# Kernel tuning notes

Hardware: AMD Instinct MI355X
Metric: run time of the kernel (lower is better)

The kernel has to match this reference:

```python
import jax, jax.numpy as jnp
import numpy as np

B, S, IN, H, E, OUT = 64, 2048, 256, 512, 256, 32000


def setup_inputs() -> dict:
    key = jax.random.key(0)
    ks = jax.random.split(key, 20)
    g = lambda k, shp, fan_in: jax.random.normal(k, shp, jnp.float32) / jnp.sqrt(jnp.float32(fan_in))
    return {
        "x": jax.random.normal(ks[0], (B, IN), jnp.float32),
        "hidden": jax.random.normal(ks[1], (B, H), jnp.float32),
        "encoder_outputs": jax.random.normal(ks[2], (B, S, H), jnp.float32),
        # attention params
        "W1_w": g(ks[3], (H, E), H), "W1_b": jnp.zeros((E,), jnp.float32),
        "W2_w": g(ks[4], (H, E), H),
        "v_w": g(ks[5], (E, 1), E),
        # GRU gate params (input to gates is concat(x, context): IN+H)
        "Wxr_w": g(ks[6], (IN + H, H), IN + H), "Wxr_b": jnp.zeros((H,), jnp.float32),
        "Whr_w": g(ks[7], (H, H), H),
        "Wxz_w": g(ks[8], (IN + H, H), IN + H), "Wxz_b": jnp.zeros((H,), jnp.float32),
        "Whz_w": g(ks[9], (H, H), H),
        "Wxh_w": g(ks[10], (IN + H, H), IN + H), "Wxh_b": jnp.zeros((H,), jnp.float32),
        "Whh_w": g(ks[11], (H, H), H),
        # output projection
        "Who_w": g(ks[12], (H, OUT), H), "Who_b": jnp.zeros((OUT,), jnp.float32),
    }


def reference(x, hidden, encoder_outputs,
              W1_w, W1_b, W2_w, v_w,
              Wxr_w, Wxr_b, Whr_w,
              Wxz_w, Wxz_b, Whz_w,
              Wxh_w, Wxh_b, Whh_w,
              Who_w, Who_b):
    # Bahdanau attention
    # energy: [B, S, E]
    energy = jnp.tanh(jnp.einsum("bsh,he->bse", encoder_outputs, W1_w) + W1_b
                      + (hidden @ W2_w)[:, None, :])
    scores = jnp.einsum("bse,eo->bs", energy, v_w)          # [B, S]
    attn_weights = jax.nn.softmax(scores, axis=1)            # [B, S]
    context = jnp.einsum("bs,bsh->bh", attn_weights, encoder_outputs)  # [B, H]

    x_context = jnp.concatenate([x, context], axis=-1)       # [B, IN+H]
    reset_gate = jax.nn.sigmoid(x_context @ Wxr_w + Wxr_b + hidden @ Whr_w)
    update_gate = jax.nn.sigmoid(x_context @ Wxz_w + Wxz_b + hidden @ Whz_w)
    h_tilde = jnp.tanh(x_context @ Wxh_w + Wxh_b + (reset_gate * hidden) @ Whh_w)
    new_hidden = update_gate * hidden + (1.0 - update_gate) * h_tilde
    output = new_hidden @ Who_w + Who_b                      # [B, OUT]
    return (output, new_hidden, attn_weights)
```

## Files before the change

### kernel.cpp

```cpp
#include <hip/hip_runtime.h>

#define BB 64
#define SS 2048
#define INDIM 256
#define HH 512
#define EE 256
#define OUTD 32000

typedef __attribute__((ext_vector_type(8))) short short8;
typedef __attribute__((ext_vector_type(4))) float floatx4;

#define LOG2E 1.4426950408889634f

__device__ __forceinline__ unsigned short f2bf(float f) {
  unsigned u = __float_as_uint(f);
  return (unsigned short)((u + 0x7FFFu + ((u >> 16) & 1u)) >> 16);
}
__device__ __forceinline__ unsigned pk2(float a, float b) {
  return (unsigned)f2bf(a) | ((unsigned)f2bf(b) << 16);
}
__device__ __forceinline__ float bf2f(unsigned short u) {
  return __uint_as_float((unsigned)u << 16);
}
__device__ __forceinline__ float fast_tanh(float x) {
  float e = __builtin_amdgcn_exp2f(x * 2.8853900817779268f);
  return 1.0f - 2.0f * __builtin_amdgcn_rcpf(e + 1.0f);
}
__device__ __forceinline__ float fast_sigmoid(float x) {
  float e = __builtin_amdgcn_exp2f(-x * LOG2E);
  return __builtin_amdgcn_rcpf(1.0f + e);
}

#define WS_W1T   0
#define WS_HBP   262144
#define WS_CTX   393216
#define WS_NHBF  524288
#define WS_Z     589824
#define WS_RH    720896
#define WS_GP    851968
#define WS_NP    3473408
#define WS_CTXP  4784128
#define WS_SUMP  38338560

__global__ void k_prep(const float* __restrict__ W1, unsigned short* __restrict__ W1t) {
  int idx = blockIdx.x * 256 + threadIdx.x;
  int k = idx >> 8, e = idx & 255;
  W1t[e * HH + k] = f2bf(W1[idx]);
}

__global__ __launch_bounds__(256) void k_hb(const float* __restrict__ hidden,
                                            const float* __restrict__ W2,
                                            const float* __restrict__ W1b,
                                            float* __restrict__ hbp) {
  int b0 = blockIdx.x * 4, seg = blockIdx.y, e = threadIdx.x;
  int h0 = seg * 256;
  float a0 = 0, a1 = 0, a2 = 0, a3 = 0;
  if (seg == 0) { a0 = a1 = a2 = a3 = W1b[e]; }
  for (int h = 0; h < 256; ++h) {
    float w = W2[(h0 + h) * EE + e];
    a0 += hidden[(b0 + 0) * HH + h0 + h] * w;
    a1 += hidden[(b0 + 1) * HH + h0 + h] * w;
    a2 += hidden[(b0 + 2) * HH + h0 + h] * w;
    a3 += hidden[(b0 + 3) * HH + h0 + h] * w;
  }
  float* o = hbp + (size_t)seg * BB * EE;
  o[(b0 + 0) * EE + e] = a0; o[(b0 + 1) * EE + e] = a1;
  o[(b0 + 2) * EE + e] = a2; o[(b0 + 3) * EE + e] = a3;
}

#define LDA 520
__global__ __launch_bounds__(256, 4) void k_scores(
    const float* __restrict__ enc, const unsigned short* __restrict__ W1t,
    const float* __restrict__ hbp, const float* __restrict__ vw,
    float* __restrict__ attn, float* __restrict__ ctxp, float* __restrict__ sump) {
  __shared__ unsigned short Afull[32 * LDA];
  __shared__ float hb_s[EE], v_s[EE];
  __shared__ float red[4 * 32];
  __shared__ float wbuf[32];

  int tid = threadIdx.x;
  int m0 = blockIdx.x * 32;
  int b = blockIdx.x >> 6;
  int sloc = (blockIdx.x & 63) * 32;
  hb_s[tid] = hbp[b * EE + tid] + hbp[BB * EE + b * EE + tid];
  v_s[tid] = vw[tid];

  int lane = tid & 63, wn = tid >> 6;
  int l15 = lane & 15, quad = lane >> 4;

  int row0 = tid >> 3, kg = tid & 7;
  const float* base0 = enc + (size_t)(m0 + row0) * HH + kg * 4;

  floatx4 acc[2][4];
#pragma unroll
  for (int i = 0; i < 2; ++i)
#pragma unroll
    for (int j = 0; j < 4; ++j) acc[i][j] = (floatx4)0.0f;

  float4 pf[6];
#pragma unroll
  for (int d = 0; d < 6; ++d) pf[d] = *(const float4*)(base0 + d * 32);

  short8 bcur[4];
#pragma unroll
  for (int j = 0; j < 4; ++j)
    bcur[j] = *(const short8*)(W1t + (wn * 64 + j * 16 + l15) * HH + quad * 8);

#pragma unroll
  for (int kb = 0; kb < 16; ++kb) {
    int slot = kb % 6;
    {
      float4 f = pf[slot];
      uint2 w; w.x = pk2(f.x, f.y); w.y = pk2(f.z, f.w);
      *(uint2*)(Afull + row0 * LDA + kb * 32 + kg * 4) = w;
    }
    if (kb + 6 < 16) pf[slot] = *(const float4*)(base0 + (kb + 6) * 32);
    short8 bnx[4];
    if (kb + 1 < 16) {
      int kkn = (kb + 1) * 32 + quad * 8;
#pragma unroll
      for (int j = 0; j < 4; ++j)
        bnx[j] = *(const short8*)(W1t + (wn * 64 + j * 16 + l15) * HH + kkn);
    }
    asm volatile("s_waitcnt lgkmcnt(0)" ::: "memory");
    __builtin_amdgcn_s_barrier();
    int kk = kb * 32 + quad * 8;
    short8 a0v = *(const short8*)(Afull + l15 * LDA + kk);
    short8 a1v = *(const short8*)(Afull + (16 + l15) * LDA + kk);
#pragma unroll
    for (int j = 0; j < 4; ++j) {
      acc[0][j] = __builtin_amdgcn_mfma_f32_16x16x32_bf16(a0v, bcur[j], acc[0][j], 0, 0, 0);
      acc[1][j] = __builtin_amdgcn_mfma_f32_16x16x32_bf16(a1v, bcur[j], acc[1][j], 0, 0, 0);
    }
    if (kb + 1 < 16) {
#pragma unroll
      for (int j = 0; j < 4; ++j) bcur[j] = bnx[j];
    }
  }
  __syncthreads();

#pragma unroll
  for (int i = 0; i < 2; ++i)
#pragma unroll
    for (int r = 0; r < 4; ++r) {
      float s = 0.0f;
#pragma unroll
      for (int j = 0; j < 4; ++j) {
        int e = wn * 64 + j * 16 + l15;
        s += fast_tanh(acc[i][j][r] + hb_s[e]) * v_s[e];
      }
#pragma unroll
      for (int off = 1; off < 16; off <<= 1) s += __shfl_xor(s, off, 64);
      if (l15 == 0) red[wn * 32 + i * 16 + quad * 4 + r] = s;
    }
  __syncthreads();
  if (tid < 32) {
    float sc = red[tid] + red[32 + tid] + red[64 + tid] + red[96 + tid];
    float e = __builtin_amdgcn_exp2f(sc * LOG2E);
    wbuf[tid] = e;
    attn[b * SS + sloc + tid] = e;
    float s = e;
#pragma unroll
    for (int off = 1; off < 32; off <<= 1) s += __shfl_xor(s, off, 64);
    if (tid == 0) sump[blockIdx.x] = s;
  }
  __syncthreads();

  float cacc[8];
#pragma unroll
  for (int j = 0; j < 8; ++j) cacc[j] = 0.0f;
#pragma unroll
  for (int rr = 0; rr < 8; ++rr) {
    int r = wn * 8 + rr;
    float w = wbuf[r];
    short8 av = *(const short8*)(Afull + r * LDA + lane * 8);
#pragma unroll
    for (int j = 0; j < 8; ++j) cacc[j] += w * bf2f((unsigned short)av[j]);
  }
  float4 c0, c1;
  c0.x = cacc[0]; c0.y = cacc[1]; c0.z = cacc[2]; c0.w = cacc[3];
  c1.x = cacc[4]; c1.y = cacc[5]; c1.z = cacc[6]; c1.w = cacc[7];
  float* cp = ctxp + ((size_t)blockIdx.x * 4 + wn) * HH + lane * 8;
  *(float4*)cp = c0;
  *(float4*)(cp + 4) = c1;
}

__global__ __launch_bounds__(512) void k_norm(float* __restrict__ attn,
                                              const float* __restrict__ ctxp,
                                              const float* __restrict__ sump,
                                              float* __restrict__ ctx) {
  int b = blockIdx.x, tid = threadIdx.x;
  float s = 0.0f;
#pragma unroll
  for (int t = 0; t < 64; ++t) s += sump[b * 64 + t];
  float inv = 1.0f / s;
#pragma unroll
  for (int i = 0; i < 4; ++i) attn[b * SS + tid + i * 512] *= inv;
  float c = 0.0f;
#pragma unroll 8
  for (int t = 0; t < 256; ++t) c += ctxp[(size_t)(b * 256 + t) * HH + tid];
  ctx[b * HH + tid] = c * inv;
}

__device__ __forceinline__ void part_seg(
    const float* __restrict__ Wx, const float* __restrict__ Wh,
    const float* __restrict__ x, const float* __restrict__ ctx,
    const float* __restrict__ hv, int seg, int b0, int h,
    float* __restrict__ outp) {
  const float* wseg;
  const float* a0; const float* a1; const float* a2; const float* a3;
  int vk0 = seg * 128;
  if (seg < 2) {
    wseg = Wx + (size_t)vk0 * HH;
    a0 = x + (b0 + 0) * INDIM + vk0;       a1 = x + (b0 + 1) * INDIM + vk0;
    a2 = x + (b0 + 2) * INDIM + vk0;       a3 = x + (b0 + 3) * INDIM + vk0;
  } else if (seg < 6) {
    wseg = Wx + (size_t)vk0 * HH;
    int off = vk0 - 256;
    a0 = ctx + (b0 + 0) * HH + off;        a1 = ctx + (b0 + 1) * HH + off;
    a2 = ctx + (b0 + 2) * HH + off;        a3 = ctx + (b0 + 3) * HH + off;
  } else {
    int off = vk0 - 768;
    wseg = Wh + (size_t)off * HH;
    a0 = hv + (b0 + 0) * HH + off;         a1 = hv + (b0 + 1) * HH + off;
    a2 = hv + (b0 + 2) * HH + off;         a3 = hv + (b0 + 3) * HH + off;
  }
  float s0 = 0, s1 = 0, s2 = 0, s3 = 0;
  for (int i = 0; i < 128; ++i) {
    float w = wseg[i * HH + h];
    s0 += a0[i] * w; s1 += a1[i] * w;
    s2 += a2[i] * w; s3 += a3[i] * w;
  }
  outp[(b0 + 0) * HH + h] = s0; outp[(b0 + 1) * HH + h] = s1;
  outp[(b0 + 2) * HH + h] = s2; outp[(b0 + 3) * HH + h] = s3;
}

__global__ __launch_bounds__(512) void k_gpart(
    const float* __restrict__ x, const float* __restrict__ ctx,
    const float* __restrict__ hidden,
    const float* __restrict__ Wxr, const float* __restrict__ Whr,
    const float* __restrict__ Wxz, const float* __restrict__ Whz,
    float* __restrict__ gp) {
  int b0 = blockIdx.x * 4, seg = blockIdx.y, sel = blockIdx.z, h = threadIdx.x;
  const float* Wx = sel ? Wxz : Wxr;
  const float* Wh = sel ? Whz : Whr;
  float* outp = gp + (size_t)(sel * 10 + seg) * BB * HH;
  part_seg(Wx, Wh, x, ctx, hidden, seg, b0, h, outp);
}

__global__ __launch_bounds__(512) void k_gred(
    const float* __restrict__ gp, const float* __restrict__ Wxrb,
    const float* __restrict__ Wxzb, const float* __restrict__ hidden,
    float* __restrict__ z_out, float* __restrict__ rh_out) {
  int b = blockIdx.x, h = threadIdx.x;
  float r = Wxrb[h], z = Wxzb[h];
#pragma unroll
  for (int s = 0; s < 10; ++s) {
    r += gp[((size_t)s * BB + b) * HH + h];
    z += gp[((size_t)(10 + s) * BB + b) * HH + h];
  }
  r = fast_sigmoid(r);
  z_out[b * HH + h] = fast_sigmoid(z);
  rh_out[b * HH + h] = r * hidden[b * HH + h];
}

__global__ __launch_bounds__(512) void k_npart(
    const float* __restrict__ x, const float* __restrict__ ctx,
    const float* __restrict__ rh,
    const float* __restrict__ Wxh, const float* __restrict__ Whh,
    float* __restrict__ np) {
  int b0 = blockIdx.x * 4, seg = blockIdx.y, h = threadIdx.x;
  float* outp = np + (size_t)seg * BB * HH;
  part_seg(Wxh, Whh, x, ctx, rh, seg, b0, h, outp);
}

__global__ __launch_bounds__(512) void k_nred(
    const float* __restrict__ np, const float* __restrict__ Wxhb,
    const float* __restrict__ z, const float* __restrict__ hidden,
    float* __restrict__ nh, unsigned short* __restrict__ nhbf) {
  int b = blockIdx.x, h = threadIdx.x;
  float a = Wxhb[h];
#pragma unroll
  for (int s = 0; s < 10; ++s) a += np[((size_t)s * BB + b) * HH + h];
  float ht = fast_tanh(a);
  float zz = z[b * HH + h];
  float val = zz * hidden[b * HH + h] + (1.0f - zz) * ht;
  nh[b * HH + h] = val;
  nhbf[b * HH + h] = f2bf(val);
}

__global__ __launch_bounds__(256) void k_out2(const unsigned short* __restrict__ nhbf,
                                              const float* __restrict__ Who,
                                              const float* __restrict__ Whob,
                                              float* __restrict__ out) {
  int tid = threadIdx.x;
  int lane = tid & 63, w = tid >> 6;
  int l15 = lane & 15, quad = lane >> 4;
  int n = blockIdx.x * 64 + w * 16 + l15;

  floatx4 acc[4];
#pragma unroll
  for (int i = 0; i < 4; ++i) acc[i] = (floatx4)0.0f;

#pragma unroll
  for (int kc = 0; kc < 16; ++kc) {
    int k0 = kc * 32;
    float bf[8];
    const float* bp = Who + (size_t)(k0 + quad * 8) * OUTD + n;
#pragma unroll
    for (int j = 0; j < 8; ++j) bf[j] = bp[(size_t)j * OUTD];
    union { unsigned u[4]; short8 v; } bu;
#pragma unroll
    for (int j = 0; j < 4; ++j) bu.u[j] = pk2(bf[2 * j], bf[2 * j + 1]);
#pragma unroll
    for (int i = 0; i < 4; ++i) {
      short8 af = *(const short8*)(nhbf + (i * 16 + l15) * HH + k0 + quad * 8);
      acc[i] = __builtin_amdgcn_mfma_f32_16x16x32_bf16(af, bu.v, acc[i], 0, 0, 0);
    }
  }
  float bias = Whob[n];
#pragma unroll
  for (int i = 0; i < 4; ++i)
#pragma unroll
    for (int r = 0; r < 4; ++r) {
      int m = i * 16 + quad * 4 + r;
      out[(size_t)m * OUTD + n] = acc[i][r] + bias;
    }
}

extern "C" void kernel_launch(void* const* d_in, const int* in_sizes, int n_in,
                              void* d_out, int out_size, void* d_ws, size_t ws_size,
                              hipStream_t stream) {
  const float* x    = (const float*)d_in[0];
  const float* hid  = (const float*)d_in[1];
  const float* enc  = (const float*)d_in[2];
  const float* W1w  = (const float*)d_in[3];
  const float* W1b  = (const float*)d_in[4];
  const float* W2w  = (const float*)d_in[5];
  const float* vw   = (const float*)d_in[6];
  const float* Wxr  = (const float*)d_in[7];
  const float* Wxrb = (const float*)d_in[8];
  const float* Whr  = (const float*)d_in[9];
  const float* Wxz  = (const float*)d_in[10];
  const float* Wxzb = (const float*)d_in[11];
  const float* Whz  = (const float*)d_in[12];
  const float* Wxh  = (const float*)d_in[13];
  const float* Wxhb = (const float*)d_in[14];
  const float* Whh  = (const float*)d_in[15];
  const float* Who  = (const float*)d_in[16];
  const float* Whob = (const float*)d_in[17];

  float* out  = (float*)d_out;
  float* nh   = out + (size_t)BB * OUTD;
  float* attn = nh + (size_t)BB * HH;

  char* ws = (char*)d_ws;
  unsigned short* W1t  = (unsigned short*)(ws + WS_W1T);
  float* hbp  = (float*)(ws + WS_HBP);
  float* ctx  = (float*)(ws + WS_CTX);
  unsigned short* nhbf = (unsigned short*)(ws + WS_NHBF);
  float* zg   = (float*)(ws + WS_Z);
  float* rh   = (float*)(ws + WS_RH);
  float* gp   = (float*)(ws + WS_GP);
  float* np   = (float*)(ws + WS_NP);
  float* ctxp = (float*)(ws + WS_CTXP);
  float* sump = (float*)(ws + WS_SUMP);

  k_prep<<<512, 256, 0, stream>>>(W1w, W1t);
  k_hb<<<dim3(16, 2), 256, 0, stream>>>(hid, W2w, W1b, hbp);
  k_scores<<<(BB * SS) / 32, 256, 0, stream>>>(enc, W1t, hbp, vw, attn, ctxp, sump);
  k_norm<<<BB, 512, 0, stream>>>(attn, ctxp, sump, ctx);
  k_gpart<<<dim3(16, 10, 2), 512, 0, stream>>>(x, ctx, hid, Wxr, Whr, Wxz, Whz, gp);
  k_gred<<<BB, 512, 0, stream>>>(gp, Wxrb, Wxzb, hid, zg, rh);
  k_npart<<<dim3(16, 10), 512, 0, stream>>>(x, ctx, rh, Wxh, Whh, np);
  k_nred<<<BB, 512, 0, stream>>>(np, Wxhb, zg, hid, nh, nhbf);
  k_out2<<<500, 256, 0, stream>>>(nhbf, Who, Whob, out);
}
```

Baseline: 608.9 us.

## Stage encoder tiles into LDS via direct global-to-LDS DMA with 512 threads

The scores kernel now loads the fp32 encoder tile straight into swizzled LDS with global_load_lds, replacing register prefetch followed by bf16 conversion stores. Block size doubles to 512 threads, each wave covering 32 energy columns, and A fragments are converted to bf16 at read time. Context partials are reduced inside the block, so ctxp shrinks fourfold and k_norm sums 64 partials per row instead of 256. The cost is 64KB of fp32 LDS per block, which lowers occupancy, and B fragments are loaded from global memory with no prefetch.

```diff
diff --git a/kernel.cpp b/kernel.cpp
--- a/kernel.cpp
+++ b/kernel.cpp
@@ -29,6 +29,12 @@
 __device__ __forceinline__ float fast_sigmoid(float x) {
   float e = __builtin_amdgcn_exp2f(-x * LOG2E);
   return __builtin_amdgcn_rcpf(1.0f + e);
+}
+
+typedef __attribute__((address_space(1))) const void g1void;
+typedef __attribute__((address_space(3))) void l3void;
+__device__ __forceinline__ void dma16(const void* g, void* l) {
+  __builtin_amdgcn_global_load_lds((g1void*)g, (l3void*)l, 16, 0, 0);
 }
 
 #define WS_W1T   0
@@ -40,7 +46,7 @@
 #define WS_GP    851968
 #define WS_NP    3473408
 #define WS_CTXP  4784128
-#define WS_SUMP  38338560
+#define WS_SUMP  21561344
 
 __global__ void k_prep(const float* __restrict__ W1, unsigned short* __restrict__ W1t) {
   int idx = blockIdx.x * 256 + threadIdx.x;
@@ -68,94 +74,85 @@
   o[(b0 + 2) * EE + e] = a2; o[(b0 + 3) * EE + e] = a3;
 }
 
-#define LDA 520
-__global__ __launch_bounds__(256, 4) void k_scores(
+__global__ __launch_bounds__(512, 4) void k_scores(
     const float* __restrict__ enc, const unsigned short* __restrict__ W1t,
     const float* __restrict__ hbp, const float* __restrict__ vw,
     float* __restrict__ attn, float* __restrict__ ctxp, float* __restrict__ sump) {
-  __shared__ unsigned short Afull[32 * LDA];
+  __shared__ float Af[32 * 512];
   __shared__ float hb_s[EE], v_s[EE];
-  __shared__ float red[4 * 32];
+  __shared__ float red[8 * 32];
   __shared__ float wbuf[32];
 
   int tid = threadIdx.x;
   int m0 = blockIdx.x * 32;
   int b = blockIdx.x >> 6;
   int sloc = (blockIdx.x & 63) * 32;
-  hb_s[tid] = hbp[b * EE + tid] + hbp[BB * EE + b * EE + tid];
-  v_s[tid] = vw[tid];
-
   int lane = tid & 63, wn = tid >> 6;
   int l15 = lane & 15, quad = lane >> 4;
 
-  int row0 = tid >> 3, kg = tid & 7;
-  const float* base0 = enc + (size_t)(m0 + row0) * HH + kg * 4;
-
-  floatx4 acc[2][4];
-#pragma unroll
-  for (int i = 0; i < 2; ++i)
-#pragma unroll
-    for (int j = 0; j < 4; ++j) acc[i][j] = (floatx4)0.0f;
-
-  float4 pf[6];
-#pragma unroll
-  for (int d = 0; d < 6; ++d) pf[d] = *(const float4*)(base0 + d * 32);
-
-  short8 bcur[4];
-#pragma unroll
-  for (int j = 0; j < 4; ++j)
-    bcur[j] = *(const short8*)(W1t + (wn * 64 + j * 16 + l15) * HH + quad * 8);
-
+#pragma unroll
+  for (int rr = 0; rr < 4; ++rr) {
+    int r = wn * 4 + rr;
+    const float* gsrc = enc + (size_t)(m0 + r) * HH + ((lane ^ (r & 7)) << 2);
+    char* ldst = (char*)Af + r * 2048;
+    dma16(gsrc, ldst);
+    dma16(gsrc + 256, ldst + 1024);
+  }
+  if (tid < 256) {
+    hb_s[tid] = hbp[b * EE + tid] + hbp[BB * EE + b * EE + tid];
+    v_s[tid] = vw[tid];
+  }
+  __syncthreads();
+
+  floatx4 acc[2][2];
+#pragma unroll
+  for (int mi = 0; mi < 2; ++mi)
+#pragma unroll
+    for (int j = 0; j < 2; ++j) acc[mi][j] = (floatx4)0.0f;
+
+  const unsigned short* bbase = W1t + (size_t)(wn * 32) * HH;
 #pragma unroll
   for (int kb = 0; kb < 16; ++kb) {
-    int slot = kb % 6;
-    {
-      float4 f = pf[slot];
-      uint2 w; w.x = pk2(f.x, f.y); w.y = pk2(f.z, f.w);
-      *(uint2*)(Afull + row0 * LDA + kb * 32 + kg * 4) = w;
-    }
-    if (kb + 6 < 16) pf[slot] = *(const float4*)(base0 + (kb + 6) * 32);
-    short8 bnx[4];
-    if (kb + 1 < 16) {
-      int kkn = (kb + 1) * 32 + quad * 8;
-#pragma unroll
-      for (int j = 0; j < 4; ++j)
-        bnx[j] = *(const short8*)(W1t + (wn * 64 + j * 16 + l15) * HH + kkn);
-    }
-    asm volatile("s_waitcnt lgkmcnt(0)" ::: "memory");
-    __builtin_amdgcn_s_barrier();
-    int kk = kb * 32 + quad * 8;
-    short8 a0v = *(const short8*)(Afull + l15 * LDA + kk);
-    short8 a1v = *(const short8*)(Afull + (16 + l15) * LDA + kk);
-#pragma unroll
-    for (int j = 0; j < 4; ++j) {
-      acc[0][j] = __builtin_amdgcn_mfma_f32_16x16x32_bf16(a0v, bcur[j], acc[0][j], 0, 0, 0);
-      acc[1][j] = __builtin_amdgcn_mfma_f32_16x16x32_bf16(a1v, bcur[j], acc[1][j], 0, 0, 0);
-    }
-    if (kb + 1 < 16) {
-#pragma unroll
-      for (int j = 0; j < 4; ++j) bcur[j] = bnx[j];
-    }
-  }
-  __syncthreads();
-
-#pragma unroll
-  for (int i = 0; i < 2; ++i)
+    short8 a[2];
+#pragma unroll
+    for (int mi = 0; mi < 2; ++mi) {
+      int r = mi * 16 + l15;
+      int s0 = kb * 8 + quad * 2;
+      const char* base = (const char*)Af + r * 2048;
+      float4 f0 = *(const float4*)(base + ((s0) ^ (l15 & 7)) * 16);
+      float4 f1 = *(const float4*)(base + ((s0 + 1) ^ (l15 & 7)) * 16);
+      union { unsigned u[4]; short8 v; } au;
+      au.u[0] = pk2(f0.x, f0.y); au.u[1] = pk2(f0.z, f0.w);
+      au.u[2] = pk2(f1.x, f1.y); au.u[3] = pk2(f1.z, f1.w);
+      a[mi] = au.v;
+    }
+#pragma unroll
+    for (int j = 0; j < 2; ++j) {
+      short8 bfr = *(const short8*)(bbase + (size_t)(j * 16 + l15) * HH + kb * 32 + quad * 8);
+      acc[0][j] = __builtin_amdgcn_mfma_f32_16x16x32_bf16(a[0], bfr, acc[0][j], 0, 0, 0);
+      acc[1][j] = __builtin_amdgcn_mfma_f32_16x16x32_bf16(a[1], bfr, acc[1][j], 0, 0, 0);
+    }
+  }
+
+#pragma unroll
+  for (int mi = 0; mi < 2; ++mi)
 #pragma unroll
     for (int r = 0; r < 4; ++r) {
       float s = 0.0f;
 #pragma unroll
-      for (int j = 0; j < 4; ++j) {
-        int e = wn * 64 + j * 16 + l15;
-        s += fast_tanh(acc[i][j][r] + hb_s[e]) * v_s[e];
+      for (int j = 0; j < 2; ++j) {
+        int e = wn * 32 + j * 16 + l15;
+        s += fast_tanh(acc[mi][j][r] + hb_s[e]) * v_s[e];
       }
 #pragma unroll
       for (int off = 1; off < 16; off <<= 1) s += __shfl_xor(s, off, 64);
-      if (l15 == 0) red[wn * 32 + i * 16 + quad * 4 + r] = s;
+      if (l15 == 0) red[wn * 32 + mi * 16 + quad * 4 + r] = s;
     }
   __syncthreads();
   if (tid < 32) {
-    float sc = red[tid] + red[32 + tid] + red[64 + tid] + red[96 + tid];
+    float sc = 0.0f;
+#pragma unroll
+    for (int w = 0; w < 8; ++w) sc += red[w * 32 + tid];
     float e = __builtin_amdgcn_exp2f(sc * LOG2E);
     wbuf[tid] = e;
     attn[b * SS + sloc + tid] = e;
@@ -166,23 +163,28 @@
   }
   __syncthreads();
 
-  float cacc[8];
-#pragma unroll
-  for (int j = 0; j < 8; ++j) cacc[j] = 0.0f;
-#pragma unroll
-  for (int rr = 0; rr < 8; ++rr) {
-    int r = wn * 8 + rr;
+  float c0[4] = {0, 0, 0, 0}, c1[4] = {0, 0, 0, 0};
+#pragma unroll
+  for (int rr = 0; rr < 4; ++rr) {
+    int r = wn * 4 + rr;
     float w = wbuf[r];
-    short8 av = *(const short8*)(Afull + r * LDA + lane * 8);
-#pragma unroll
-    for (int j = 0; j < 8; ++j) cacc[j] += w * bf2f((unsigned short)av[j]);
-  }
-  float4 c0, c1;
-  c0.x = cacc[0]; c0.y = cacc[1]; c0.z = cacc[2]; c0.w = cacc[3];
-  c1.x = cacc[4]; c1.y = cacc[5]; c1.z = cacc[6]; c1.w = cacc[7];
-  float* cp = ctxp + ((size_t)blockIdx.x * 4 + wn) * HH + lane * 8;
-  *(float4*)cp = c0;
-  *(float4*)(cp + 4) = c1;
+    const char* base = (const char*)Af + r * 2048;
+    float4 f0 = *(const float4*)(base + (lane ^ (r & 7)) * 16);
+    float4 f1 = *(const float4*)(base + 1024 + (lane ^ (r & 7)) * 16);
+    c0[0] += w * f0.x; c0[1] += w * f0.y; c0[2] += w * f0.z; c0[3] += w * f0.w;
+    c1[0] += w * f1.x; c1[1] += w * f1.y; c1[2] += w * f1.z; c1[3] += w * f1.w;
+  }
+  __syncthreads();
+  float* scr = (float*)Af;
+  float4 s0; s0.x = c0[0]; s0.y = c0[1]; s0.z = c0[2]; s0.w = c0[3];
+  float4 s1; s1.x = c1[0]; s1.y = c1[1]; s1.z = c1[2]; s1.w = c1[3];
+  *(float4*)(scr + wn * 512 + lane * 4) = s0;
+  *(float4*)(scr + wn * 512 + 256 + lane * 4) = s1;
+  __syncthreads();
+  float c = 0.0f;
+#pragma unroll
+  for (int w = 0; w < 8; ++w) c += scr[w * 512 + tid];
+  ctxp[(size_t)blockIdx.x * HH + tid] = c;
 }
 
 __global__ __launch_bounds__(512) void k_norm(float* __restrict__ attn,
@@ -198,7 +200,7 @@
   for (int i = 0; i < 4; ++i) attn[b * SS + tid + i * 512] *= inv;
   float c = 0.0f;
 #pragma unroll 8
-  for (int t = 0; t < 256; ++t) c += ctxp[(size_t)(b * 256 + t) * HH + tid];
+  for (int t = 0; t < 64; ++t) c += ctxp[(size_t)(b * 64 + t) * HH + tid];
   ctx[b * HH + tid] = c * inv;
 }
 
@@ -368,7 +370,7 @@
 
   k_prep<<<512, 256, 0, stream>>>(W1w, W1t);
   k_hb<<<dim3(16, 2), 256, 0, stream>>>(hid, W2w, W1b, hbp);
-  k_scores<<<(BB * SS) / 32, 256, 0, stream>>>(enc, W1t, hbp, vw, attn, ctxp, sump);
+  k_scores<<<(BB * SS) / 32, 512, 0, stream>>>(enc, W1t, hbp, vw, attn, ctxp, sump);
   k_norm<<<BB, 512, 0, stream>>>(attn, ctxp, sump, ctx);
   k_gpart<<<dim3(16, 10, 2), 512, 0, stream>>>(x, ctx, hid, Wxr, Whr, Wxz, Whz, gp);
   k_gred<<<BB, 512, 0, stream>>>(gp, Wxrb, Wxzb, hid, zg, rh);
```

Result: faster. 589.7 us (-3.1%).
